# Kernel optimization log

Hardware: AMD Instinct MI355X
Metric: run time of the kernel (lower is better)

## Reference

```python
import jax, jax.numpy as jnp
import numpy as np
from jax import lax

SQRT_HALF = 0.7071067811865476
LAYERS = 20
STACKS = 2
LAYERS_PER_STACK = LAYERS // STACKS
K = 3
OUT_CH = 256
RES_CH = 64
GATE_CH = 128
SKIP_CH = 256
CIN_CH = 80


def setup_inputs() -> dict:
    key = jax.random.key(0)
    ks = jax.random.split(key, 20)
    s = 0.05
    inp = {
        'x': jax.random.normal(ks[0], (4, OUT_CH, 16384), jnp.float32),
        'c': jax.random.normal(ks[1], (4, CIN_CH, 16384), jnp.float32),
        # first conv: kernel size 2 (Conv1d2x1), out_channels -> residual_channels
        'W_first': jax.random.normal(ks[2], (RES_CH, OUT_CH, 2), jnp.float32) * s,
        'b_first': jnp.zeros((RES_CH,), jnp.float32),
        # per-layer dilated conv (residual -> gate), stacked over layers
        'W_dil': jax.random.normal(ks[3], (LAYERS, GATE_CH, RES_CH, K), jnp.float32) * s,
        'b_dil': jnp.zeros((LAYERS, GATE_CH), jnp.float32),
        # per-layer local-conditioning 1x1 (cin -> gate)
        'W_c': jax.random.normal(ks[4], (LAYERS, GATE_CH, CIN_CH), jnp.float32) * s,
        'b_c': jnp.zeros((LAYERS, GATE_CH), jnp.float32),
        # per-layer 1x1 skip (gate/2 -> skip) and out (gate/2 -> residual)
        'W_skip': jax.random.normal(ks[5], (LAYERS, SKIP_CH, GATE_CH // 2), jnp.float32) * s,
        'b_skip': jnp.zeros((LAYERS, SKIP_CH), jnp.float32),
        'W_out': jax.random.normal(ks[6], (LAYERS, RES_CH, GATE_CH // 2), jnp.float32) * s,
        'b_out': jnp.zeros((LAYERS, RES_CH), jnp.float32),
        # final 1x1 convs
        'W_last1': jax.random.normal(ks[7], (SKIP_CH, SKIP_CH), jnp.float32) * s,
        'b_last1': jnp.zeros((SKIP_CH,), jnp.float32),
        'W_last2': jax.random.normal(ks[8], (OUT_CH, SKIP_CH), jnp.float32) * s,
        'b_last2': jnp.zeros((OUT_CH,), jnp.float32),
    }
    return inp


def reference(x, c, W_first, b_first, W_dil, b_dil, W_c, b_c,
              W_skip, b_skip, W_out, b_out, W_last1, b_last1, W_last2, b_last2):
    dn = ('NCH', 'OIH', 'NCH')
    # first conv: F.pad(x, (1,0)) then kernel-2 conv == causal left pad 1
    h = lax.conv_general_dilated(x, W_first, (1,), [(1, 0)], dimension_numbers=dn)
    h = jnp.tanh(h + b_first[None, :, None])  # hparams.use_tanh_embed
    skips = None
    for l in range(LAYERS):
        d = 2 ** (l % LAYERS_PER_STACK)
        # causal dilated conv: pad left (K-1)*d
        y = lax.conv_general_dilated(h, W_dil[l], (1,), [((K - 1) * d, 0)],
                                     rhs_dilation=(d,), dimension_numbers=dn)
        y = y + b_dil[l][None, :, None]
        cond = jnp.einsum('bct,gc->bgt', c, W_c[l]) + b_c[l][None, :, None]
        a, b = jnp.split(y + cond, 2, axis=1)  # gated activation units
        z = jnp.tanh(a) * jax.nn.sigmoid(b)
        s = jnp.einsum('bgt,sg->bst', z, W_skip[l]) + b_skip[l][None, :, None]
        h = (jnp.einsum('bgt,rg->brt', z, W_out[l]) + b_out[l][None, :, None] + h) * SQRT_HALF
        if skips is None:
            skips = s
        else:
            skips = (skips + s) * SQRT_HALF  # faithful to original accumulation
    out = jax.nn.relu(skips)
    out = jnp.einsum('bst,os->bot', out, W_last1) + b_last1[None, :, None]
    out = jax.nn.relu(out)
    out = jnp.einsum('bst,os->bot', out, W_last2) + b_last2[None, :, None]
    return out
```

## Files before the change

### kernel.cpp

```cpp
#include <hip/hip_runtime.h>
#include <math.h>


#define T_LEN   16384
#define NB      4
#define BT      (NB * T_LEN)
#define NLAYERS 20
#define SQH     0.70710678118654752440f

typedef _Float16 half8 __attribute__((ext_vector_type(8)));
typedef _Float16 half4 __attribute__((ext_vector_type(4)));
typedef float f32x4 __attribute__((ext_vector_type(4)));

__device__ inline f32x4 mfma16(half8 a, half8 b, f32x4 c) {
  return __builtin_amdgcn_mfma_f32_16x16x32_f16(a, b, c, 0, 0, 0);
}

__device__ __forceinline__ int xswz(int pb, int nwg) {
  return (pb & 7) * (nwg >> 3) + (pb >> 3);
}

__global__ __launch_bounds__(256) void prep_pack(
    const float* __restrict__ Wf, const float* __restrict__ Wdil,
    const float* __restrict__ Wc, const float* __restrict__ Wskip,
    const float* __restrict__ Wout, const float* __restrict__ Wl1,
    const float* __restrict__ Wl2, const float* __restrict__ bdil,
    const float* __restrict__ bc, const float* __restrict__ bskip,
    _Float16* __restrict__ wdp, _Float16* __restrict__ wcp,
    _Float16* __restrict__ wop, _Float16* __restrict__ wskp,
    _Float16* __restrict__ wfp, _Float16* __restrict__ wl1p,
    _Float16* __restrict__ wl2p, float* __restrict__ bde,
    float* __restrict__ bsk)
{
  const float Q = 0.70710678118654752440f;
  const int WDP_E = 20 * 3 * 128 * 64;
  const int WCP_E = 20 * 128 * 96;
  const int WOP_E = 20 * 64 * 64;
  const int WSK_E = 256 * 1280;
  const int WFP_E = 64 * 512;
  const int WL_E  = 256 * 256;
  const int BDE_E = 20 * 128;
  const int BSK_E = 256;
  const int TOTAL = WDP_E + WCP_E + WOP_E + WSK_E + WFP_E + 2 * WL_E + BDE_E + BSK_E;
  for (int i = blockIdx.x * blockDim.x + threadIdx.x; i < TOTAL;
       i += gridDim.x * blockDim.x) {
    int j = i;
    if (j < WDP_E) {
      int l = j / (3 * 128 * 64); int r2 = j % (3 * 128 * 64);
      int tau = r2 / (128 * 64);  int r3 = r2 % (128 * 64);
      int n = r3 >> 6; int kc = r3 & 63;
      wdp[j] = (_Float16)Wdil[((l * 128 + n) * 64 + kc) * 3 + tau];
      continue;
    }
    j -= WDP_E;
    if (j < WCP_E) {
      int l = j / (128 * 96); int r2 = j % (128 * 96);
      int n = r2 / 96; int kc = r2 % 96;
      wcp[j] = (_Float16)(kc < 80 ? Wc[(l * 128 + n) * 80 + kc] : 0.f);
      continue;
    }
    j -= WCP_E;
    if (j < WOP_E) {
      int l = j >> 12; int r2 = j & 4095;
      int n = r2 >> 6; int kc = r2 & 63;
      wop[j] = (_Float16)Wout[(l * 64 + n) * 64 + kc];
      continue;
    }
    j -= WOP_E;
    if (j < WSK_E) {
      int n = j / 1280; int k = j % 1280;
      int l = k >> 6; int kc = k & 63;
      float f = (l == 0) ? 1.f : powf(Q, (float)(1 - l));
      wskp[j] = (_Float16)(Wskip[(l * 256 + n) * 64 + kc] * f);
      continue;
    }
    j -= WSK_E;
    if (j < WFP_E) {
      int n = j >> 9; int k = j & 511;
      int tau = k >> 8; int ci = k & 255;
      wfp[j] = (_Float16)Wf[(n * 256 + ci) * 2 + tau];
      continue;
    }
    j -= WFP_E;
    if (j < WL_E) { wl1p[j] = (_Float16)Wl1[j]; continue; }
    j -= WL_E;
    if (j < WL_E) { wl2p[j] = (_Float16)Wl2[j]; continue; }
    j -= WL_E;
    if (j < BDE_E) { bde[j] = bdil[j] + bc[j]; continue; }
    j -= BDE_E;
    {
      int n = j;
      float s = 0.f;
      for (int l = 0; l < NLAYERS; ++l) {
        float w = powf(Q, (float)(l == 0 ? 19 : 20 - l));
        s += bskip[l * 256 + n] * w;
      }
      bsk[n] = s;
    }
  }
}

__global__ __launch_bounds__(256) void tr_x_kernel(
    const float* __restrict__ src, _Float16* __restrict__ dst)
{
  __shared__ float tile[32 * 132];
  const int lb = xswz(blockIdx.x, 4096);
  const int row_tile = lb >> 3, cb = lb & 7;
  const int bb = row_tile >> 7;
  const int t0 = (row_tile & 127) * 128;
  const int ch0 = cb * 32;
  {
    int ch = threadIdx.x >> 3, tq = (threadIdx.x & 7) * 16;
    const float4* s4 = (const float4*)(src + ((size_t)(bb * 256 + ch0 + ch)) * T_LEN + t0 + tq);
#pragma unroll
    for (int j = 0; j < 4; ++j)
      *(float4*)&tile[ch * 132 + tq + 4 * j] = s4[j];
  }
  __syncthreads();
  {
    int t = threadIdx.x >> 1, c16 = (threadIdx.x & 1) * 16;
    half8 h0, h1;
#pragma unroll
    for (int j = 0; j < 8; ++j) {
      h0[j] = (_Float16)tile[(c16 + j) * 132 + t];
      h1[j] = (_Float16)tile[(c16 + 8 + j) * 132 + t];
    }
    _Float16* o = dst + ((size_t)(bb * T_LEN + t0 + t)) * 256 + ch0 + c16;
    *(half8*)o = h0;
    *(half8*)(o + 8) = h1;
  }
}

__global__ __launch_bounds__(256) void tr_kernel(
    const float* __restrict__ src, _Float16* __restrict__ dst, int C, int Cpad, int CB)
{
  __shared__ float tile[32 * 33];
  int lb = xswz(blockIdx.x, gridDim.x);
  int cb = lb % CB;
  int tb = (lb / CB) % (T_LEN / 32);
  int bb = lb / (CB * (T_LEN / 32));
  int t0 = tb * 32, ch0 = cb * 32;
  int tl = threadIdx.x & 31, cl = threadIdx.x >> 5;
#pragma unroll
  for (int i = 0; i < 4; ++i) {
    int ch = cl + 8 * i;
    float v = (ch0 + ch < C) ? src[((size_t)bb * C + ch0 + ch) * T_LEN + t0 + tl] : 0.f;
    tile[ch * 33 + tl] = v;
  }
  __syncthreads();
  int t = threadIdx.x >> 3;
  int c4 = (threadIdx.x & 7) * 4;
  half4 hv = {(_Float16)tile[(c4 + 0) * 33 + t], (_Float16)tile[(c4 + 1) * 33 + t],
              (_Float16)tile[(c4 + 2) * 33 + t], (_Float16)tile[(c4 + 3) * 33 + t]};
  *(half4*)&dst[((size_t)bb * T_LEN + t0 + t) * Cpad + ch0 + c4] = hv;
}

__global__ __launch_bounds__(256, 4) void first_conv(
    const _Float16* __restrict__ xt, const _Float16* __restrict__ wfp,
    const float* __restrict__ bf, _Float16* __restrict__ h0)
{
  __shared__ _Float16 As[128 * 72];
  __shared__ _Float16 Bs[64 * 72];
  const int tid = threadIdx.x;
  const int lane = tid & 63, w = tid >> 6;
  const int wx = w & 1, wy = w >> 1;
  const int l15 = lane & 15, quad = lane >> 4;
  const int p0 = xswz(blockIdx.x, 512) * 128;
  const int b = p0 >> 14, t0 = p0 & (T_LEN - 1);
  const int r = tid >> 1, halfo = (tid & 1) * 32;

  f32x4 acc[4][2];
#pragma unroll
  for (int mi = 0; mi < 4; ++mi)
#pragma unroll
    for (int ni = 0; ni < 2; ++ni) { f32x4 z = {0.f, 0.f, 0.f, 0.f}; acc[mi][ni] = z; }

  for (int s = 0; s < 8; ++s) {
    int tau = s >> 2, ci0 = (s & 3) * 64;
    int ts = t0 + r - 1 + tau;
    if (ts >= 0) {
      const uint4* src = (const uint4*)(xt + ((size_t)(b * T_LEN + ts) * 256 + ci0 + halfo));
#pragma unroll
      for (int j = 0; j < 4; ++j) *(uint4*)&As[r * 72 + halfo + 8 * j] = src[j];
    } else {
      uint4 z = {0, 0, 0, 0};
#pragma unroll
      for (int j = 0; j < 4; ++j) *(uint4*)&As[r * 72 + halfo + 8 * j] = z;
    }
    if (tid < 128) {
      const uint4* s4 = (const uint4*)(wfp + ((size_t)r * 512 + tau * 256 + ci0 + halfo));
#pragma unroll
      for (int j = 0; j < 4; ++j) *(uint4*)&Bs[r * 72 + halfo + 8 * j] = s4[j];
    }
    __syncthreads();
#pragma unroll
    for (int kc = 0; kc < 2; ++kc) {
      const int k0 = kc * 32 + quad * 8;
      half8 af[4], bfr[2];
#pragma unroll
      for (int mi = 0; mi < 4; ++mi)
        af[mi] = *(const half8*)&As[(64 * wy + 16 * mi + l15) * 72 + k0];
#pragma unroll
      for (int ni = 0; ni < 2; ++ni)
        bfr[ni] = *(const half8*)&Bs[(32 * wx + 16 * ni + l15) * 72 + k0];
#pragma unroll
      for (int mi = 0; mi < 4; ++mi)
#pragma unroll
        for (int ni = 0; ni < 2; ++ni)
          acc[mi][ni] = mfma16(af[mi], bfr[ni], acc[mi][ni]);
    }
    __syncthreads();
  }
#pragma unroll
  for (int mi = 0; mi < 4; ++mi)
#pragma unroll
    for (int ni = 0; ni < 2; ++ni) {
      int col = 32 * wx + 16 * ni + l15;
      int rowb = 64 * wy + 16 * mi + quad * 4;
      float bo = bf[col];
#pragma unroll
      for (int reg = 0; reg < 4; ++reg) {
        float v = acc[mi][ni][reg] + bo;
        float e = __expf(2.f * v);
        As[(rowb + reg) * 72 + col] = (_Float16)(1.f - 2.f * __builtin_amdgcn_rcpf(e + 1.f));
      }
    }
  __syncthreads();
  {
    int row = tid >> 1, co = (tid & 1) * 32;
    _Float16* o = h0 + ((size_t)(p0 + row)) * 64 + co;
    const uint4* s = (const uint4*)&As[row * 72 + co];
#pragma unroll
    for (int j = 0; j < 4; ++j) *(uint4*)(o + 8 * j) = s[j];
  }
}

__global__ __launch_bounds__(512, 4) void layer_kernel(
    const _Float16* __restrict__ hprev, _Float16* __restrict__ hnext,
    const _Float16* __restrict__ ctp,
    const _Float16* __restrict__ wdp_l, const _Float16* __restrict__ wcp_l,
    const _Float16* __restrict__ wop_l,
    const float* __restrict__ bde_l, const float* __restrict__ bout_l,
    _Float16* __restrict__ zslot, int d, int last)
{
  __shared__ _Float16 As[128 * 72];
  __shared__ _Float16 Bs[128 * 72];
  __shared__ float bde_s[128];

  const int tid = threadIdx.x;
  const int lane = tid & 63, w = tid >> 6;
  const int wx = w & 1, wy = w >> 1;
  const int l15 = lane & 15, quad = lane >> 4;
  const int p0 = xswz(blockIdx.x, 512) * 128;
  const int b = p0 >> 14, t0 = p0 & (T_LEN - 1);
  const int r2 = tid >> 2, qo = (tid & 3) * 16;
  const int o8 = (tid & 3) * 8;

  if (tid < 128) bde_s[tid] = bde_l[tid];

  f32x4 acc[2][4];
#pragma unroll
  for (int mi = 0; mi < 2; ++mi)
#pragma unroll
    for (int ni = 0; ni < 4; ++ni) { f32x4 z = {0.f, 0.f, 0.f, 0.f}; acc[mi][ni] = z; }

  for (int s = 0; s < 5; ++s) {
    if (s < 3) {
      int ts = t0 + r2 - (2 - s) * d;
      if (ts >= 0) {
        const uint4* src = (const uint4*)(hprev + ((size_t)(b * T_LEN + ts) * 64 + qo));
        *(uint4*)&As[r2 * 72 + qo] = src[0];
        *(uint4*)&As[r2 * 72 + qo + 8] = src[1];
      } else {
        uint4 z4 = {0, 0, 0, 0};
        *(uint4*)&As[r2 * 72 + qo] = z4;
        *(uint4*)&As[r2 * 72 + qo + 8] = z4;
      }
      const uint4* sb = (const uint4*)(wdp_l + ((size_t)s * 8192 + r2 * 64 + qo));
      *(uint4*)&Bs[r2 * 72 + qo] = sb[0];
      *(uint4*)&Bs[r2 * 72 + qo + 8] = sb[1];
    } else if (s == 3) {
      const uint4* sa = (const uint4*)(ctp + ((size_t)(p0 + r2) * 96 + qo));
      *(uint4*)&As[r2 * 72 + qo] = sa[0];
      *(uint4*)&As[r2 * 72 + qo + 8] = sa[1];
      const uint4* sb = (const uint4*)(wcp_l + ((size_t)r2 * 96 + qo));
      *(uint4*)&Bs[r2 * 72 + qo] = sb[0];
      *(uint4*)&Bs[r2 * 72 + qo + 8] = sb[1];
    } else {
      *(uint4*)&As[r2 * 72 + o8] = *(const uint4*)(ctp + ((size_t)(p0 + r2) * 96 + 64 + o8));
      *(uint4*)&Bs[r2 * 72 + o8] = *(const uint4*)(wcp_l + ((size_t)r2 * 96 + 64 + o8));
    }
    __syncthreads();
    const int nkc = (s == 4) ? 1 : 2;
    for (int kc = 0; kc < nkc; ++kc) {
      const int k0 = kc * 32 + quad * 8;
      half8 af[2], bfr[4];
#pragma unroll
      for (int mi = 0; mi < 2; ++mi)
        af[mi] = *(const half8*)&As[(32 * wy + 16 * mi + l15) * 72 + k0];
#pragma unroll
      for (int ni = 0; ni < 4; ++ni) {
        int ncol = 32 * wx + 16 * (ni & 1) + 64 * (ni >> 1);
        bfr[ni] = *(const half8*)&Bs[(ncol + l15) * 72 + k0];
      }
#pragma unroll
      for (int mi = 0; mi < 2; ++mi)
#pragma unroll
        for (int ni = 0; ni < 4; ++ni)
          acc[mi][ni] = mfma16(af[mi], bfr[ni], acc[mi][ni]);
    }
    __syncthreads();
  }

#pragma unroll
  for (int mi = 0; mi < 2; ++mi)
#pragma unroll
    for (int ni2 = 0; ni2 < 2; ++ni2) {
      int colb = 32 * wx + 16 * ni2 + l15;
      float ba = bde_s[colb], bb = bde_s[colb + 64];
#pragma unroll
      for (int reg = 0; reg < 4; ++reg) {
        float av = acc[mi][ni2][reg] + ba;
        float gv = acc[mi][ni2 + 2][reg] + bb;
        float ea = __expf(2.f * av);
        float th = 1.f - 2.f * __builtin_amdgcn_rcpf(ea + 1.f);
        float sg = __builtin_amdgcn_rcpf(1.f + __expf(-gv));
        As[(32 * wy + 16 * mi + quad * 4 + reg) * 72 + colb] = (_Float16)(th * sg);
      }
    }

  if (!last && tid < 256) {
    int row = tid >> 2;
    const uint4* sb = (const uint4*)(wop_l + ((size_t)row * 64 + qo));
    *(uint4*)&Bs[row * 72 + qo] = sb[0];
    *(uint4*)&Bs[row * 72 + qo + 8] = sb[1];
  }
  __syncthreads();

  {
    uint4 v0 = *(const uint4*)&As[r2 * 72 + qo];
    uint4 v1 = *(const uint4*)&As[r2 * 72 + qo + 8];
    uint4* dst = (uint4*)(zslot + ((size_t)(p0 + r2) * 64 + qo));
    dst[0] = v0; dst[1] = v1;
  }

  if (last) return;

  f32x4 a4[2][2];
#pragma unroll
  for (int mi = 0; mi < 2; ++mi)
#pragma unroll
    for (int ni = 0; ni < 2; ++ni) { f32x4 z = {0.f, 0.f, 0.f, 0.f}; a4[mi][ni] = z; }
#pragma unroll
  for (int kc = 0; kc < 2; ++kc) {
    const int k0 = kc * 32 + quad * 8;
    half8 af[2], bfr[2];
#pragma unroll
    for (int mi = 0; mi < 2; ++mi)
      af[mi] = *(const half8*)&As[(32 * wy + 16 * mi + l15) * 72 + k0];
#pragma unroll
    for (int ni = 0; ni < 2; ++ni)
      bfr[ni] = *(const half8*)&Bs[(32 * wx + 16 * ni + l15) * 72 + k0];
#pragma unroll
    for (int mi = 0; mi < 2; ++mi)
#pragma unroll
      for (int ni = 0; ni < 2; ++ni)
        a4[mi][ni] = mfma16(af[mi], bfr[ni], a4[mi][ni]);
  }
  __syncthreads();
#pragma unroll
  for (int mi = 0; mi < 2; ++mi)
#pragma unroll
    for (int ni = 0; ni < 2; ++ni) {
      int col = 32 * wx + 16 * ni + l15;
      int rowb = 32 * wy + 16 * mi + quad * 4;
      float bo = bout_l[col];
      size_t base = ((size_t)p0 + rowb) * 64 + col;
#pragma unroll
      for (int reg = 0; reg < 4; ++reg) {
        float hv = (float)hprev[base + (size_t)64 * reg];
        As[(rowb + reg) * 72 + col] = (_Float16)((a4[mi][ni][reg] + bo + hv) * SQH);
      }
    }
  __syncthreads();
  {
    uint4 v0 = *(const uint4*)&As[r2 * 72 + qo];
    uint4 v1 = *(const uint4*)&As[r2 * 72 + qo + 8];
    uint4* dst = (uint4*)(hnext + ((size_t)(p0 + r2) * 64 + qo));
    dst[0] = v0; dst[1] = v1;
  }
}

__global__ __launch_bounds__(512, 4) void flush_kernel(
    const _Float16* __restrict__ zbuf, const _Float16* __restrict__ wskp,
    _Float16* __restrict__ Abuf, const float* __restrict__ bsk,
    _Float16* __restrict__ skr, int l0, int g, int mode)
{
  __shared__ _Float16 As[128 * 72];
  __shared__ _Float16 Bs0[128 * 72];
  __shared__ _Float16 Bs1[128 * 72];
  const int tid = threadIdx.x;
  const int half = tid >> 8;
  _Float16* Bsh = half ? Bs1 : Bs0;
  const int tloc = tid & 255;
  const int lane = tloc & 63, w4 = tloc >> 6;
  const int wx = w4 & 1, wy = w4 >> 1;
  const int l15 = lane & 15, quad = lane >> 4;
  const int p0 = xswz(blockIdx.x, 512) * 128;
  const int n0 = half * 128;
  const int r = tloc >> 1, halfo = (tloc & 1) * 32;

  f32x4 acc[4][4];
#pragma unroll
  for (int mi = 0; mi < 4; ++mi)
#pragma unroll
    for (int ni = 0; ni < 4; ++ni) { f32x4 z = {0.f, 0.f, 0.f, 0.f}; acc[mi][ni] = z; }

#pragma unroll 1
  for (int j = 0; j < g; ++j) {
    const int lj = l0 + j;
    const _Float16* zsl = zbuf + (size_t)(lj & 7) * ((size_t)BT * 64);
    if (half == 0) {
      const uint4* sa = (const uint4*)(zsl + ((size_t)(p0 + r) * 64 + halfo));
#pragma unroll
      for (int jj = 0; jj < 4; ++jj) *(uint4*)&As[r * 72 + halfo + 8 * jj] = sa[jj];
    }
    const uint4* sb = (const uint4*)(wskp + ((size_t)(n0 + r) * 1280 + lj * 64 + halfo));
#pragma unroll
    for (int jj = 0; jj < 4; ++jj) *(uint4*)&Bsh[r * 72 + halfo + 8 * jj] = sb[jj];
    __syncthreads();
#pragma unroll
    for (int kc = 0; kc < 2; ++kc) {
      const int k0 = kc * 32 + quad * 8;
      half8 af[4], bfr[4];
#pragma unroll
      for (int mi = 0; mi < 4; ++mi)
        af[mi] = *(const half8*)&As[(64 * wy + 16 * mi + l15) * 72 + k0];
#pragma unroll
      for (int ni = 0; ni < 4; ++ni)
        bfr[ni] = *(const half8*)&Bsh[(64 * wx + 16 * ni + l15) * 72 + k0];
#pragma unroll
      for (int mi = 0; mi < 4; ++mi)
#pragma unroll
        for (int ni = 0; ni < 4; ++ni)
          acc[mi][ni] = mfma16(af[mi], bfr[ni], acc[mi][ni]);
    }
    __syncthreads();
  }
  const float Q19 = 0.0013810679320049757f;
#pragma unroll
  for (int mi = 0; mi < 4; ++mi)
#pragma unroll
    for (int ni = 0; ni < 4; ++ni) {
      int col = n0 + 64 * wx + 16 * ni + l15;
      int rowb = 64 * wy + 16 * mi + quad * 4;
      size_t base = ((size_t)p0 + rowb) * 256 + col;
      if (mode == 2) {
        float bb = bsk[col];
#pragma unroll
        for (int reg = 0; reg < 4; ++reg) {
          float v = (acc[mi][ni][reg] + (float)Abuf[base + (size_t)256 * reg]) * Q19 + bb;
          skr[base + (size_t)256 * reg] = (_Float16)(v > 0.f ? v : 0.f);
        }
      } else if (mode == 1) {
#pragma unroll
        for (int reg = 0; reg < 4; ++reg) {
          size_t a = base + (size_t)256 * reg;
          Abuf[a] = (_Float16)((float)Abuf[a] + acc[mi][ni][reg]);
        }
      } else {
#pragma unroll
        for (int reg = 0; reg < 4; ++reg)
          Abuf[base + (size_t)256 * reg] = (_Float16)acc[mi][ni][reg];
      }
    }
}

__global__ __launch_bounds__(256, 4) void gemm256(
    const _Float16* __restrict__ Asrc, const _Float16* __restrict__ Bp,
    const float* __restrict__ bias, void* __restrict__ dst, int mode)
{
  __shared__ _Float16 smem[2 * 128 * 72];
  _Float16* As = smem;
  _Float16* Bs = smem + 128 * 72;
  const int tid = threadIdx.x;
  const int lane = tid & 63, w = tid >> 6;
  const int wx = w & 1, wy = w >> 1;
  const int l15 = lane & 15, quad = lane >> 4;
  const int p0 = xswz(blockIdx.x, 512) * 128;
  const int n0 = blockIdx.y * 128;
  const int r = tid >> 1, halfo = (tid & 1) * 32;

  f32x4 acc[4][4];
#pragma unroll
  for (int mi = 0; mi < 4; ++mi)
#pragma unroll
    for (int ni = 0; ni < 4; ++ni) { f32x4 z = {0.f, 0.f, 0.f, 0.f}; acc[mi][ni] = z; }

  for (int c4 = 0; c4 < 4; ++c4) {
    int k0g = c4 * 64;
    const uint4* sa = (const uint4*)(Asrc + ((size_t)(p0 + r) * 256 + k0g + halfo));
#pragma unroll
    for (int jj = 0; jj < 4; ++jj) *(uint4*)&As[r * 72 + halfo + 8 * jj] = sa[jj];
    const uint4* sb = (const uint4*)(Bp + ((size_t)(n0 + r) * 256 + k0g + halfo));
#pragma unroll
    for (int jj = 0; jj < 4; ++jj) *(uint4*)&Bs[r * 72 + halfo + 8 * jj] = sb[jj];
    __syncthreads();
#pragma unroll
    for (int kc = 0; kc < 2; ++kc) {
      const int k0 = kc * 32 + quad * 8;
      half8 af[4], bfr[4];
#pragma unroll
      for (int mi = 0; mi < 4; ++mi)
        af[mi] = *(const half8*)&As[(64 * wy + 16 * mi + l15) * 72 + k0];
#pragma unroll
      for (int ni = 0; ni < 4; ++ni)
        bfr[ni] = *(const half8*)&Bs[(64 * wx + 16 * ni + l15) * 72 + k0];
#pragma unroll
      for (int mi = 0; mi < 4; ++mi)
#pragma unroll
        for (int ni = 0; ni < 4; ++ni)
          acc[mi][ni] = mfma16(af[mi], bfr[ni], acc[mi][ni]);
    }
    __syncthreads();
  }
  if (mode == 0) {
    _Float16* Ts = smem;
#pragma unroll 1
    for (int h = 0; h < 2; ++h) {
      if (wy == h) {
#pragma unroll
        for (int mi = 0; mi < 4; ++mi)
#pragma unroll
          for (int ni = 0; ni < 4; ++ni) {
            int col = 64 * wx + 16 * ni + l15;
            int lr = 16 * mi + quad * 4;
            float bv = bias[n0 + col];
#pragma unroll
            for (int reg = 0; reg < 4; ++reg) {
              float v = acc[mi][ni][reg] + bv;
              Ts[(lr + reg) * 136 + col] = (_Float16)(v > 0.f ? v : 0.f);
            }
          }
      }
      __syncthreads();
      {
        int lr = tid >> 2, co = (tid & 3) * 32;
        _Float16* o = (_Float16*)dst + ((size_t)(p0 + 64 * h + lr)) * 256 + n0 + co;
        const uint4* s = (const uint4*)&Ts[lr * 136 + co];
#pragma unroll
        for (int jj = 0; jj < 4; ++jj) *(uint4*)(o + 8 * jj) = s[jj];
      }
      __syncthreads();
    }
  } else {
    float* Ts = (float*)smem;
    const int b = p0 >> 14, t0g = p0 & (T_LEN - 1);
    for (int pass = 0; pass < 2; ++pass) {
      if (wx == pass) {
#pragma unroll
        for (int mi = 0; mi < 4; ++mi)
#pragma unroll
          for (int ni = 0; ni < 4; ++ni) {
            int col_l = 16 * ni + l15;
            float bv = bias[n0 + 64 * pass + col_l];
            int tl = 64 * wy + 16 * mi + quad * 4;
#pragma unroll
            for (int reg = 0; reg < 4; ++reg)
              Ts[col_l * 132 + tl + reg] = acc[mi][ni][reg] + bv;
          }
      }
      __syncthreads();
      {
        int col_l = tid >> 2;
        int tq = (tid & 3) * 32;
        float* o = (float*)dst + ((size_t)b * 256 + n0 + 64 * pass + col_l) * T_LEN + t0g + tq;
#pragma unroll
        for (int j = 0; j < 8; ++j)
          *(float4*)(o + 4 * j) = *(const float4*)&Ts[col_l * 132 + tq + 4 * j];
      }
      __syncthreads();
    }
  }
}

extern "C" void kernel_launch(void* const* d_in, const int* in_sizes, int n_in,
                              void* d_out, int out_size, void* d_ws, size_t ws_size,
                              hipStream_t stream)
{
  const float* x     = (const float*)d_in[0];
  const float* c     = (const float*)d_in[1];
  const float* Wf    = (const float*)d_in[2];
  const float* bf    = (const float*)d_in[3];
  const float* Wdil  = (const float*)d_in[4];
  const float* bdil  = (const float*)d_in[5];
  const float* Wc    = (const float*)d_in[6];
  const float* bc    = (const float*)d_in[7];
  const float* Wskip = (const float*)d_in[8];
  const float* bskip = (const float*)d_in[9];
  const float* Wout  = (const float*)d_in[10];
  const float* bout  = (const float*)d_in[11];
  const float* Wl1   = (const float*)d_in[12];
  const float* bl1   = (const float*)d_in[13];
  const float* Wl2   = (const float*)d_in[14];
  const float* bl2   = (const float*)d_in[15];

  char* base = (char*)d_ws;
  _Float16* zbuf = (_Float16*)base;
  _Float16* xt   = zbuf;
  _Float16* skr  = zbuf + (size_t)4 * BT * 64;
  _Float16* y1   = zbuf;
  _Float16* ctp  = (_Float16*)(base + 67108864);
  _Float16* hA   = (_Float16*)(base + 79691776);
  _Float16* hB   = (_Float16*)(base + 88080384);
  _Float16* wdp  = (_Float16*)(base + 96468992);
  _Float16* wcp  = wdp  + (size_t)20 * 3 * 128 * 64;
  _Float16* wop  = wcp  + (size_t)20 * 128 * 96;
  _Float16* wskp = wop  + (size_t)20 * 64 * 64;
  _Float16* wfp  = wskp + (size_t)256 * 1280;
  _Float16* wl1p = wfp  + (size_t)64 * 512;
  _Float16* wl2p = wl1p + (size_t)256 * 256;
  float*    bde  = (float*)(wl2p + (size_t)256 * 256);
  float*    bsk  = bde + 20 * 128;
  _Float16* Abuf = (_Float16*)d_out;

  prep_pack<<<2048, 256, 0, stream>>>(Wf, Wdil, Wc, Wskip, Wout, Wl1, Wl2,
                                      bdil, bc, bskip,
                                      wdp, wcp, wop, wskp, wfp, wl1p, wl2p,
                                      bde, bsk);
  tr_x_kernel<<<4096, 256, 0, stream>>>(x, xt);
  tr_kernel<<<NB * (T_LEN / 32) * 3, 256, 0, stream>>>(c, ctp, 80, 96, 3);
  first_conv<<<512, 256, 0, stream>>>(xt, wfp, bf, hA);

  const _Float16* hin = hA;
  _Float16* hout = hB;
  for (int l = 0; l < NLAYERS; ++l) {
    int d = 1 << (l % 10);
    layer_kernel<<<512, 512, 0, stream>>>(
        hin, hout, ctp,
        wdp + (size_t)l * 3 * 128 * 64, wcp + (size_t)l * 128 * 96,
        wop + (size_t)l * 64 * 64, bde + l * 128, bout + l * 64,
        zbuf + (size_t)(l & 7) * BT * 64, d, (l == NLAYERS - 1) ? 1 : 0);
    _Float16* tmp = (_Float16*)hin; hin = hout; hout = tmp;
    if (l == 7)  flush_kernel<<<512, 512, 0, stream>>>(zbuf, wskp, Abuf, bsk, skr, 0, 8, 0);
    if (l == 15) flush_kernel<<<512, 512, 0, stream>>>(zbuf, wskp, Abuf, bsk, skr, 8, 8, 1);
    if (l == 19) flush_kernel<<<512, 512, 0, stream>>>(zbuf, wskp, Abuf, bsk, skr, 16, 4, 2);
  }
  gemm256<<<dim3(512, 2), 256, 0, stream>>>(skr, wl1p, bl1, (void*)y1, 0);
  gemm256<<<dim3(512, 2), 256, 0, stream>>>(y1, wl2p, bl2, d_out, 1);
}
```

Baseline: 625.7 us.

## Merge prologue kernels and overlap skip flushes with layer kernels

Three prologue launches (weight packing, x transpose, c transpose) become one kernel that picks its role from the block index. Skip-projection flushes now run inside the same launch as layers 7, 14 and 19, with blocks interleaved so the flush GEMM overlaps with layer compute. A small final flush then handles layer 19's z. The fused kernel raises shared memory per block and lowers launch bounds to 2 blocks per CU, which can cut occupancy for the layer blocks it shares a launch with.

```diff
diff --git a/kernel.cpp b/kernel.cpp
--- a/kernel.cpp
+++ b/kernel.cpp
@@ -20,18 +20,75 @@
   return (pb & 7) * (nwg >> 3) + (pb >> 3);
 }
 
-__global__ __launch_bounds__(256) void prep_pack(
+__global__ __launch_bounds__(256) void prologue_kernel(
+    const float* __restrict__ x, const float* __restrict__ c,
     const float* __restrict__ Wf, const float* __restrict__ Wdil,
     const float* __restrict__ Wc, const float* __restrict__ Wskip,
     const float* __restrict__ Wout, const float* __restrict__ Wl1,
     const float* __restrict__ Wl2, const float* __restrict__ bdil,
     const float* __restrict__ bc, const float* __restrict__ bskip,
+    _Float16* __restrict__ xt, _Float16* __restrict__ ctp,
     _Float16* __restrict__ wdp, _Float16* __restrict__ wcp,
     _Float16* __restrict__ wop, _Float16* __restrict__ wskp,
     _Float16* __restrict__ wfp, _Float16* __restrict__ wl1p,
     _Float16* __restrict__ wl2p, float* __restrict__ bde,
     float* __restrict__ bsk)
 {
+  __shared__ float ptile[32 * 132];
+  const int pid = blockIdx.x;
+  const int tid = threadIdx.x;
+
+  if (pid < 4096) {
+    const int lb = xswz(pid, 4096);
+    const int row_tile = lb >> 3, cb = lb & 7;
+    const int bb = row_tile >> 7;
+    const int t0 = (row_tile & 127) * 128;
+    const int ch0 = cb * 32;
+    {
+      int ch = tid >> 3, tq = (tid & 7) * 16;
+      const float4* s4 = (const float4*)(x + ((size_t)(bb * 256 + ch0 + ch)) * T_LEN + t0 + tq);
+#pragma unroll
+      for (int j = 0; j < 4; ++j)
+        *(float4*)&ptile[ch * 132 + tq + 4 * j] = s4[j];
+    }
+    __syncthreads();
+    {
+      int t = tid >> 1, c16 = (tid & 1) * 16;
+      half8 h0, h1;
+#pragma unroll
+      for (int j = 0; j < 8; ++j) {
+        h0[j] = (_Float16)ptile[(c16 + j) * 132 + t];
+        h1[j] = (_Float16)ptile[(c16 + 8 + j) * 132 + t];
+      }
+      _Float16* o = xt + ((size_t)(bb * T_LEN + t0 + t)) * 256 + ch0 + c16;
+      *(half8*)o = h0;
+      *(half8*)(o + 8) = h1;
+    }
+    return;
+  }
+  if (pid < 4096 + 6144) {
+    const int pb = pid - 4096;
+    int lb = xswz(pb, 6144);
+    int cb = lb % 3;
+    int tb = (lb / 3) % (T_LEN / 32);
+    int bb = lb / (3 * (T_LEN / 32));
+    int t0 = tb * 32, ch0 = cb * 32;
+    int tl = tid & 31, cl = tid >> 5;
+#pragma unroll
+    for (int i = 0; i < 4; ++i) {
+      int ch = cl + 8 * i;
+      float v = (ch0 + ch < 80) ? c[((size_t)bb * 80 + ch0 + ch) * T_LEN + t0 + tl] : 0.f;
+      ptile[ch * 33 + tl] = v;
+    }
+    __syncthreads();
+    int t = tid >> 3;
+    int c4 = (tid & 7) * 4;
+    half4 hv = {(_Float16)ptile[(c4 + 0) * 33 + t], (_Float16)ptile[(c4 + 1) * 33 + t],
+                (_Float16)ptile[(c4 + 2) * 33 + t], (_Float16)ptile[(c4 + 3) * 33 + t]};
+    *(half4*)&ctp[((size_t)bb * T_LEN + t0 + t) * 96 + ch0 + c4] = hv;
+    return;
+  }
+  const int pid2 = pid - (4096 + 6144);
   const float Q = 0.70710678118654752440f;
   const int WDP_E = 20 * 3 * 128 * 64;
   const int WCP_E = 20 * 128 * 96;
@@ -40,10 +97,8 @@
   const int WFP_E = 64 * 512;
   const int WL_E  = 256 * 256;
   const int BDE_E = 20 * 128;
-  const int BSK_E = 256;
-  const int TOTAL = WDP_E + WCP_E + WOP_E + WSK_E + WFP_E + 2 * WL_E + BDE_E + BSK_E;
-  for (int i = blockIdx.x * blockDim.x + threadIdx.x; i < TOTAL;
-       i += gridDim.x * blockDim.x) {
+  const int TOTAL = WDP_E + WCP_E + WOP_E + WSK_E + WFP_E + 2 * WL_E + BDE_E + 256;
+  for (int i = pid2 * 256 + tid; i < TOTAL; i += 2048 * 256) {
     int j = i;
     if (j < WDP_E) {
       int l = j / (3 * 128 * 64); int r2 = j % (3 * 128 * 64);
@@ -100,61 +155,6 @@
   }
 }
 
-__global__ __launch_bounds__(256) void tr_x_kernel(
-    const float* __restrict__ src, _Float16* __restrict__ dst)
-{
-  __shared__ float tile[32 * 132];
-  const int lb = xswz(blockIdx.x, 4096);
-  const int row_tile = lb >> 3, cb = lb & 7;
-  const int bb = row_tile >> 7;
-  const int t0 = (row_tile & 127) * 128;
-  const int ch0 = cb * 32;
-  {
-    int ch = threadIdx.x >> 3, tq = (threadIdx.x & 7) * 16;
-    const float4* s4 = (const float4*)(src + ((size_t)(bb * 256 + ch0 + ch)) * T_LEN + t0 + tq);
-#pragma unroll
-    for (int j = 0; j < 4; ++j)
-      *(float4*)&tile[ch * 132 + tq + 4 * j] = s4[j];
-  }
-  __syncthreads();
-  {
-    int t = threadIdx.x >> 1, c16 = (threadIdx.x & 1) * 16;
-    half8 h0, h1;
-#pragma unroll
-    for (int j = 0; j < 8; ++j) {
-      h0[j] = (_Float16)tile[(c16 + j) * 132 + t];
-      h1[j] = (_Float16)tile[(c16 + 8 + j) * 132 + t];
-    }
-    _Float16* o = dst + ((size_t)(bb * T_LEN + t0 + t)) * 256 + ch0 + c16;
-    *(half8*)o = h0;
-    *(half8*)(o + 8) = h1;
-  }
-}
-
-__global__ __launch_bounds__(256) void tr_kernel(
-    const float* __restrict__ src, _Float16* __restrict__ dst, int C, int Cpad, int CB)
-{
-  __shared__ float tile[32 * 33];
-  int lb = xswz(blockIdx.x, gridDim.x);
-  int cb = lb % CB;
-  int tb = (lb / CB) % (T_LEN / 32);
-  int bb = lb / (CB * (T_LEN / 32));
-  int t0 = tb * 32, ch0 = cb * 32;
-  int tl = threadIdx.x & 31, cl = threadIdx.x >> 5;
-#pragma unroll
-  for (int i = 0; i < 4; ++i) {
-    int ch = cl + 8 * i;
-    float v = (ch0 + ch < C) ? src[((size_t)bb * C + ch0 + ch) * T_LEN + t0 + tl] : 0.f;
-    tile[ch * 33 + tl] = v;
-  }
-  __syncthreads();
-  int t = threadIdx.x >> 3;
-  int c4 = (threadIdx.x & 7) * 4;
-  half4 hv = {(_Float16)tile[(c4 + 0) * 33 + t], (_Float16)tile[(c4 + 1) * 33 + t],
-              (_Float16)tile[(c4 + 2) * 33 + t], (_Float16)tile[(c4 + 3) * 33 + t]};
-  *(half4*)&dst[((size_t)bb * T_LEN + t0 + t) * Cpad + ch0 + c4] = hv;
-}
-
 __global__ __launch_bounds__(256, 4) void first_conv(
     const _Float16* __restrict__ xt, const _Float16* __restrict__ wfp,
     const float* __restrict__ bf, _Float16* __restrict__ h0)
@@ -235,7 +235,8 @@
   }
 }
 
-__global__ __launch_bounds__(512, 4) void layer_kernel(
+__device__ __forceinline__ void layer_body(
+    int lb, int tid, _Float16* smem, float* bde_s,
     const _Float16* __restrict__ hprev, _Float16* __restrict__ hnext,
     const _Float16* __restrict__ ctp,
     const _Float16* __restrict__ wdp_l, const _Float16* __restrict__ wcp_l,
@@ -243,15 +244,12 @@
     const float* __restrict__ bde_l, const float* __restrict__ bout_l,
     _Float16* __restrict__ zslot, int d, int last)
 {
-  __shared__ _Float16 As[128 * 72];
-  __shared__ _Float16 Bs[128 * 72];
-  __shared__ float bde_s[128];
-
-  const int tid = threadIdx.x;
+  _Float16* As = smem;
+  _Float16* Bs = smem + 128 * 72;
   const int lane = tid & 63, w = tid >> 6;
   const int wx = w & 1, wy = w >> 1;
   const int l15 = lane & 15, quad = lane >> 4;
-  const int p0 = xswz(blockIdx.x, 512) * 128;
+  const int p0 = xswz(lb, 512) * 128;
   const int b = p0 >> 14, t0 = p0 & (T_LEN - 1);
   const int r2 = tid >> 2, qo = (tid & 3) * 16;
   const int o8 = (tid & 3) * 8;
@@ -391,22 +389,22 @@
   }
 }
 
-__global__ __launch_bounds__(512, 4) void flush_kernel(
+__device__ __forceinline__ void flush_body(
+    int fb, int tid, _Float16* smem,
     const _Float16* __restrict__ zbuf, const _Float16* __restrict__ wskp,
     _Float16* __restrict__ Abuf, const float* __restrict__ bsk,
     _Float16* __restrict__ skr, int l0, int g, int mode)
 {
-  __shared__ _Float16 As[128 * 72];
-  __shared__ _Float16 Bs0[128 * 72];
-  __shared__ _Float16 Bs1[128 * 72];
-  const int tid = threadIdx.x;
+  _Float16* As = smem;
+  _Float16* Bs0 = smem + 128 * 72;
+  _Float16* Bs1 = smem + 2 * 128 * 72;
   const int half = tid >> 8;
   _Float16* Bsh = half ? Bs1 : Bs0;
   const int tloc = tid & 255;
   const int lane = tloc & 63, w4 = tloc >> 6;
   const int wx = w4 & 1, wy = w4 >> 1;
   const int l15 = lane & 15, quad = lane >> 4;
-  const int p0 = xswz(blockIdx.x, 512) * 128;
+  const int p0 = xswz(fb, 512) * 128;
   const int n0 = half * 128;
   const int r = tloc >> 1, halfo = (tloc & 1) * 32;
 
@@ -474,6 +472,58 @@
           Abuf[base + (size_t)256 * reg] = (_Float16)acc[mi][ni][reg];
       }
     }
+}
+
+__global__ __launch_bounds__(512, 4) void layer_kernel(
+    const _Float16* __restrict__ hprev, _Float16* __restrict__ hnext,
+    const _Float16* __restrict__ ctp,
+    const _Float16* __restrict__ wdp_l, const _Float16* __restrict__ wcp_l,
+    const _Float16* __restrict__ wop_l,
+    const float* __restrict__ bde_l, const float* __restrict__ bout_l,
+    _Float16* __restrict__ zslot, int d, int last)
+{
+  __shared__ _Float16 smem[2 * 128 * 72];
+  __shared__ float bde_s[128];
+  layer_body(blockIdx.x, threadIdx.x, smem, bde_s,
+             hprev, hnext, ctp, wdp_l, wcp_l, wop_l, bde_l, bout_l,
+             zslot, d, last);
+}
+
+__global__ __launch_bounds__(512, 2) void layer_flush_kernel(
+    const _Float16* __restrict__ hprev, _Float16* __restrict__ hnext,
+    const _Float16* __restrict__ ctp,
+    const _Float16* __restrict__ wdp_l, const _Float16* __restrict__ wcp_l,
+    const _Float16* __restrict__ wop_l,
+    const float* __restrict__ bde_l, const float* __restrict__ bout_l,
+    _Float16* __restrict__ zslot, int d, int last,
+    const _Float16* __restrict__ zbuf, const _Float16* __restrict__ wskp,
+    _Float16* __restrict__ Abuf, const float* __restrict__ bsk,
+    _Float16* __restrict__ skr, int fl0, int fg, int fmode)
+{
+  __shared__ _Float16 smem[3 * 128 * 72];
+  __shared__ float bde_s[128];
+  const int p = blockIdx.x;
+  const int grp = p & 15;
+  if (grp < 8) {
+    int lb = (p >> 4) * 8 + grp;
+    layer_body(lb, threadIdx.x, smem, bde_s,
+               hprev, hnext, ctp, wdp_l, wcp_l, wop_l, bde_l, bout_l,
+               zslot, d, last);
+  } else {
+    int fb = (p >> 4) * 8 + grp - 8;
+    flush_body(fb, threadIdx.x, smem,
+               zbuf, wskp, Abuf, bsk, skr, fl0, fg, fmode);
+  }
+}
+
+__global__ __launch_bounds__(512, 4) void flush_kernel(
+    const _Float16* __restrict__ zbuf, const _Float16* __restrict__ wskp,
+    _Float16* __restrict__ Abuf, const float* __restrict__ bsk,
+    _Float16* __restrict__ skr, int l0, int g, int mode)
+{
+  __shared__ _Float16 smem[3 * 128 * 72];
+  flush_body(blockIdx.x, threadIdx.x, smem,
+             zbuf, wskp, Abuf, bsk, skr, l0, g, mode);
 }
 
 __global__ __launch_bounds__(256, 4) void gemm256(
@@ -624,28 +674,37 @@
   float*    bsk  = bde + 20 * 128;
   _Float16* Abuf = (_Float16*)d_out;
 
-  prep_pack<<<2048, 256, 0, stream>>>(Wf, Wdil, Wc, Wskip, Wout, Wl1, Wl2,
-                                      bdil, bc, bskip,
-                                      wdp, wcp, wop, wskp, wfp, wl1p, wl2p,
-                                      bde, bsk);
-  tr_x_kernel<<<4096, 256, 0, stream>>>(x, xt);
-  tr_kernel<<<NB * (T_LEN / 32) * 3, 256, 0, stream>>>(c, ctp, 80, 96, 3);
+  prologue_kernel<<<4096 + 6144 + 2048, 256, 0, stream>>>(
+      x, c, Wf, Wdil, Wc, Wskip, Wout, Wl1, Wl2, bdil, bc, bskip,
+      xt, ctp, wdp, wcp, wop, wskp, wfp, wl1p, wl2p, bde, bsk);
   first_conv<<<512, 256, 0, stream>>>(xt, wfp, bf, hA);
 
   const _Float16* hin = hA;
   _Float16* hout = hB;
   for (int l = 0; l < NLAYERS; ++l) {
     int d = 1 << (l % 10);
-    layer_kernel<<<512, 512, 0, stream>>>(
-        hin, hout, ctp,
-        wdp + (size_t)l * 3 * 128 * 64, wcp + (size_t)l * 128 * 96,
-        wop + (size_t)l * 64 * 64, bde + l * 128, bout + l * 64,
-        zbuf + (size_t)(l & 7) * BT * 64, d, (l == NLAYERS - 1) ? 1 : 0);
+    int last = (l == NLAYERS - 1) ? 1 : 0;
+    if (l == 7 || l == 14 || l == 19) {
+      int fl0 = (l == 7) ? 0 : (l == 14) ? 7 : 14;
+      int fg  = (l == 19) ? 5 : 7;
+      int fm  = (l == 7) ? 0 : 1;
+      layer_flush_kernel<<<1024, 512, 0, stream>>>(
+          hin, hout, ctp,
+          wdp + (size_t)l * 3 * 128 * 64, wcp + (size_t)l * 128 * 96,
+          wop + (size_t)l * 64 * 64, bde + l * 128, bout + l * 64,
+          zbuf + (size_t)(l & 7) * BT * 64, d, last,
+          zbuf, wskp, Abuf, bsk, skr, fl0, fg, fm);
+    } else {
+      layer_kernel<<<512, 512, 0, stream>>>(
+          hin, hout, ctp,
+          wdp + (size_t)l * 3 * 128 * 64, wcp + (size_t)l * 128 * 96,
+          wop + (size_t)l * 64 * 64, bde + l * 128, bout + l * 64,
+          zbuf + (size_t)(l & 7) * BT * 64, d, last);
+    }
     _Float16* tmp = (_Float16*)hin; hin = hout; hout = tmp;
-    if (l == 7)  flush_kernel<<<512, 512, 0, stream>>>(zbuf, wskp, Abuf, bsk, skr, 0, 8, 0);
-    if (l == 15) flush_kernel<<<512, 512, 0, stream>>>(zbuf, wskp, Abuf, bsk, skr, 8, 8, 1);
-    if (l == 19) flush_kernel<<<512, 512, 0, stream>>>(zbuf, wskp, Abuf, bsk, skr, 16, 4, 2);
-  }
+  }
+  flush_kernel<<<512, 512, 0, stream>>>(zbuf, wskp, Abuf, bsk, skr, 19, 1, 2);
+
   gemm256<<<dim3(512, 2), 256, 0, stream>>>(skr, wl1p, bl1, (void*)y1, 0);
   gemm256<<<dim3(512, 2), 256, 0, stream>>>(y1, wl2p, bl2, d_out, 1);
 }
```

Measured after the change: 670.1 us. 1.07x slower.
